# Performance work log

Measured on AMD Instinct MI355X. Metric: run time of the kernel, lower is better.

The kernel has to match this reference:

```python
import jax, jax.numpy as jnp
import numpy as np

# Video-DiT scale: d_model = H * D = 2048
B, S_T, S_C, H, D = 2, 2048, 1024, 16, 128


def setup_inputs() -> dict:
    key = jax.random.key(0)
    ks = jax.random.split(key, 6)
    f = lambda k, s: jax.random.normal(k, s, dtype=jnp.float32)
    return {
        "target_q": f(ks[0], (B, S_T, H, D)),
        "target_k": f(ks[1], (B, S_T, H, D)),
        "target_v": f(ks[2], (B, S_T, H, D)),
        "cond_k": f(ks[3], (B, S_C, H, D)),
        "cond_v": f(ks[4], (B, S_C, H, D)),
        "b_param": f(ks[5], (1,)),
    }


def reference(target_q, target_k, target_v, cond_k, cond_v, b_param):
    """Extended target self-attention over [target_k; cond_k] with a scalar
    logit bias b_param added only to the condition-key columns.
    Inputs BSHD; returns [B, S_t, H*D] (ready for output_proj)."""
    Bq, St, Hh, Dd = target_q.shape
    Sc = cond_k.shape[1]
    scale = Dd ** -0.5  # softmax_scale defaults to head_dim**-0.5

    k_ext = jnp.concatenate([target_k, cond_k], axis=1)  # [B, S_t+S_c, H, D]
    v_ext = jnp.concatenate([target_v, cond_v], axis=1)

    # [B, H, S_t, S_t+S_c]
    logits = jnp.einsum('bqhd,bkhd->bhqk', target_q, k_ext) * jnp.asarray(scale, target_q.dtype)
    # bias: 0 on target keys, b on cond keys
    bias = jnp.concatenate([
        jnp.zeros((St,), logits.dtype),
        jnp.broadcast_to(b_param.astype(logits.dtype), (Sc,)),
    ])
    logits = logits + bias[None, None, None, :]

    probs = jax.nn.softmax(logits, axis=-1)
    out = jnp.einsum('bhqk,bkhd->bqhd', probs, v_ext)  # [B, S_t, H, D]
    return out.reshape(Bq, St, Hh * Dd)
```

## Files before the change

kernel.cpp:

```cpp
#include <hip/hip_runtime.h>
#include <hip/hip_bf16.h>

typedef __attribute__((ext_vector_type(4))) float f32x4;
typedef __attribute__((ext_vector_type(16))) float f32x16;
typedef __attribute__((ext_vector_type(8))) short bf8;
typedef __attribute__((ext_vector_type(2))) int i32x2;

#define B_ 2
#define ST 2048
#define SC 1024
#define SK 3072
#define NH 16
#define DH 128
#define KVB 32
#define NT 96
#define TGT 64
#define SCALE 0.088388347648318447f
#define LOG2E 1.4426950408889634f
#define PRE_TILE_U32 2048
#define PRE_BYTES (32ull * 96 * 512 * 16)
#define WS_NEED (2ull * PRE_BYTES)

__device__ __forceinline__ i32x2 tr_read(unsigned a) {
    i32x2 d;
    asm volatile("ds_read_b64_tr_b16 %0, %1" : "=v"(d) : "v"(a));
    return d;
}

__device__ __forceinline__ unsigned cvtpk(float lo, float hi) {
    unsigned r;
    asm("v_cvt_pk_bf16_f32 %0, %1, %2" : "=v"(r) : "v"(lo), "v"(hi));
    return r;
}

__device__ __forceinline__ void swap32(unsigned &a, unsigned &b) {
    asm volatile("v_permlane32_swap_b32 %0, %1" : "+v"(a), "+v"(b));
}

__device__ __forceinline__ bf8 mk_bf8(i32x2 a, i32x2 b) {
    union { i32x2 h[2]; bf8 v; } u;
    u.h[0] = a; u.h[1] = b;
    return u.v;
}
__device__ __forceinline__ bf8 mk_bf8w(unsigned w0, unsigned w1, unsigned w2, unsigned w3) {
    union { unsigned w[4]; bf8 v; } u;
    u.w[0] = w0; u.w[1] = w1; u.w[2] = w2; u.w[3] = w3;
    return u.v;
}
__device__ __forceinline__ bf8 pack_bf8(f32x4 a, f32x4 b) {
    return mk_bf8w(cvtpk(a[0], a[1]), cvtpk(a[2], a[3]),
                   cvtpk(b[0], b[1]), cvtpk(b[2], b[3]));
}

__global__ __launch_bounds__(256)
void preconv(const float* __restrict__ TK, const float* __restrict__ TV,
             const float* __restrict__ CK, const float* __restrict__ CV,
             unsigned* __restrict__ KP, unsigned* __restrict__ VP)
{
    const unsigned gid = blockIdx.x * 256 + threadIdx.x;
    const int c    = gid & 511;
    const int idx  = gid >> 9;
    const int bhid = idx / 96;
    const int t    = idx - bhid * 96;
    const int bb   = bhid >> 4;
    const int hh   = bhid & 15;
    const int lc   = c & 63;
    const int r31c = lc & 31;
    const int hic  = lc >> 5;

    const bool tgt = (t < TGT);
    const size_t krowbase = tgt
        ? (((size_t)bb * ST + t * 32) * NH + hh) * DH
        : (((size_t)bb * SC + (t * 32 - ST)) * NH + hh) * DH;
    const float* kb = (tgt ? TK : CK) + krowbase;
    const float* vb = (tgt ? TV : CV) + krowbase;

    {
        const int dk = c >> 6;
        const float* kp = kb + (size_t)r31c * (NH * DH) + dk * 16 + hic * 8;
        const f32x4 k0 = *(const f32x4*)kp;
        const f32x4 k1 = *(const f32x4*)(kp + 4);
        unsigned* ko = KP + (size_t)gid * 4;
        ko[0] = cvtpk(k0[0], k0[1]); ko[1] = cvtpk(k0[2], k0[3]);
        ko[2] = cvtpk(k1[0], k1[1]); ko[3] = cvtpk(k1[2], k1[3]);
    }

    {
        const int s  = c >> 6;
        const int ks = s >> 2;
        const int dt = s & 3;
        const int d  = dt * 32 + r31c;
        const float* vp = vb + (size_t)(ks * 16 + hic * 8) * (NH * DH) + d;
        float vv[8];
#pragma unroll
        for (int j = 0; j < 8; ++j) vv[j] = vp[(size_t)j * (NH * DH)];
        unsigned* vo = VP + (size_t)gid * 4;
        vo[0] = cvtpk(vv[0], vv[1]); vo[1] = cvtpk(vv[2], vv[3]);
        vo[2] = cvtpk(vv[4], vv[5]); vo[3] = cvtpk(vv[6], vv[7]);
    }
}

__global__ __launch_bounds__(256) __attribute__((amdgpu_waves_per_eu(2, 2)))
void attn_fwd_pre(const float* __restrict__ Q,
                  const unsigned* __restrict__ KP,
                  const unsigned* __restrict__ VP,
                  const float* __restrict__ BP,
                  float* __restrict__ OUT)
{
    __shared__ __align__(16) unsigned short Ks[3][KVB * DH];
    __shared__ __align__(16) unsigned short Vs[3][KVB * DH];

    const int tid = threadIdx.x;
    const int w   = tid >> 6;
    const int l   = tid & 63;
    const int r31 = l & 31;
    const int hi  = l >> 5;

    const int bid = blockIdx.x;
    const int xcd = bid & 7;
    const int sub = bid >> 3;
    const int bh  = xcd * 4 + (sub >> 4);
    const int qt  = sub & 15;
    const int bb  = bh >> 4;
    const int hh  = bh & 15;
    const int bh96 = bh * 96;

    const float biasl = BP[0] * LOG2E;

    const int qrow = qt * 128 + w * 32 + r31;
    const float* qp = Q + (((size_t)bb * ST + qrow) * NH + hh) * DH;
    const float qsc = SCALE * LOG2E;
    bf8 qf[8];
#pragma unroll
    for (int dk = 0; dk < 8; ++dk) {
        const f32x4 x0 = *(const f32x4*)(qp + dk * 16 + hi * 8);
        const f32x4 x1 = *(const f32x4*)(qp + dk * 16 + hi * 8 + 4);
        qf[dk] = mk_bf8w(cvtpk(x0[0]*qsc, x0[1]*qsc), cvtpk(x0[2]*qsc, x0[3]*qsc),
                         cvtpk(x1[0]*qsc, x1[1]*qsc), cvtpk(x1[2]*qsc, x1[3]*qsc));
    }

    f32x16 oa[4];
#pragma unroll
    for (int dt = 0; dt < 4; ++dt)
#pragma unroll
        for (int e = 0; e < 16; ++e) oa[dt][e] = 0.f;
    float l_run = 0.f;

    auto stage = [&](int t, int buf) {
        const unsigned* kt = KP + (size_t)(bh96 + t) * PRE_TILE_U32;
        const unsigned* vt = VP + (size_t)(bh96 + t) * PRE_TILE_U32;
#pragma unroll
        for (int i = 0; i < 2; ++i) {
            const int cb = (w << 6) + (i << 8);
            const unsigned kdst = (unsigned)(size_t)&Ks[buf][cb * 8];
            const unsigned vdst = (unsigned)(size_t)&Vs[buf][cb * 8];
            const unsigned* kg = kt + (size_t)(cb + l) * 4;
            const unsigned* vg = vt + (size_t)(cb + l) * 4;
            __builtin_amdgcn_global_load_lds(
                (const __attribute__((address_space(1))) unsigned*)(size_t)kg,
                (__attribute__((address_space(3))) unsigned*)(size_t)kdst, 16, 0, 0);
            __builtin_amdgcn_global_load_lds(
                (const __attribute__((address_space(1))) unsigned*)(size_t)vg,
                (__attribute__((address_space(3))) unsigned*)(size_t)vdst, 16, 0, 0);
        }
    };

    const char* kLane = (const char*)&Ks[0][0] + l * 16;
    const char* vLane = (const char*)&Vs[0][0] + l * 16;

    auto qk_into = [&](f32x16& SN, int bufn, float biasn) {
#pragma unroll
        for (int e = 0; e < 16; ++e) SN[e] = biasn;
        const char* kB = kLane + (unsigned)bufn * 8192u;
        __builtin_amdgcn_s_setprio(1);
#pragma unroll
        for (int dk = 0; dk < 8; ++dk) {
            const bf8 kf = *(const bf8*)(kB + dk * 1024);
            SN = __builtin_amdgcn_mfma_f32_32x32x16_bf16(kf, qf[dk], SN, 0, 0, 0);
        }
        __builtin_amdgcn_s_setprio(0);
    };

    stage(0, 0);
    stage(1, 1);
    asm volatile("s_waitcnt vmcnt(4)" ::: "memory");
    __builtin_amdgcn_s_barrier();
    asm volatile("" ::: "memory");
    f32x16 sA, sB;
    qk_into(sA, 0, 0.f);

    int b0 = 0, b1 = 1, b2 = 2;

    auto body = [&](int t, f32x16& SCr, f32x16& SNr) {
        if (t + 1 < NT) asm volatile("s_waitcnt vmcnt(0)" ::: "memory");
        __builtin_amdgcn_s_barrier();
        asm volatile("" ::: "memory");
        if (t + 2 < NT) stage(t + 2, b2);

        if (t + 1 < NT)
            qk_into(SNr, b1, (t + 1 >= TGT) ? biasl : 0.f);

        const char* vB = vLane + (unsigned)b0 * 8192u;
        bf8 vf[8];
#pragma unroll
        for (int s = 0; s < 8; ++s)
            vf[s] = *(const bf8*)(vB + s * 1024);

        float rs = 0.f;
#pragma unroll
        for (int e = 0; e < 16; ++e) {
            SCr[e] = __builtin_amdgcn_exp2f(SCr[e]);
            rs += SCr[e];
        }
        l_run += rs;

        unsigned a0 = cvtpk(SCr[0], SCr[1]),  c0 = cvtpk(SCr[4], SCr[5]);
        unsigned a1 = cvtpk(SCr[2], SCr[3]),  c1 = cvtpk(SCr[6], SCr[7]);
        swap32(a0, c0); swap32(a1, c1);
        const bf8 pf0 = mk_bf8w(a0, a1, c0, c1);
        unsigned a2 = cvtpk(SCr[8], SCr[9]),   c2 = cvtpk(SCr[12], SCr[13]);
        unsigned a3 = cvtpk(SCr[10], SCr[11]), c3 = cvtpk(SCr[14], SCr[15]);
        swap32(a2, c2); swap32(a3, c3);
        const bf8 pf1 = mk_bf8w(a2, a3, c2, c3);

        __builtin_amdgcn_s_setprio(1);
#pragma unroll
        for (int dt = 0; dt < 4; ++dt)
            oa[dt] = __builtin_amdgcn_mfma_f32_32x32x16_bf16(vf[dt], pf0, oa[dt], 0, 0, 0);
#pragma unroll
        for (int dt = 0; dt < 4; ++dt)
            oa[dt] = __builtin_amdgcn_mfma_f32_32x32x16_bf16(vf[4 + dt], pf1, oa[dt], 0, 0, 0);
        __builtin_amdgcn_s_setprio(0);

        const int n0 = b1, n1 = b2, n2 = b0;
        b0 = n0; b1 = n1; b2 = n2;
    };

    for (int t = 0; t < NT; t += 2) {
        body(t, sA, sB);
        body(t + 1, sB, sA);
    }

    const float l_tot = l_run + __shfl_xor(l_run, 32);
    const float inv = 1.0f / l_tot;
    float* op = OUT + ((size_t)(bb * ST + qrow)) * (NH * DH) + hh * DH;
#pragma unroll
    for (int dt = 0; dt < 4; ++dt)
#pragma unroll
        for (int rr = 0; rr < 4; ++rr) {
            f32x4 st;
            st[0] = oa[dt][rr * 4 + 0] * inv;
            st[1] = oa[dt][rr * 4 + 1] * inv;
            st[2] = oa[dt][rr * 4 + 2] * inv;
            st[3] = oa[dt][rr * 4 + 3] * inv;
            *(f32x4*)(op + dt * 32 + rr * 8 + hi * 4) = st;
        }
}

__global__ __launch_bounds__(256, 2)
void attn_fwd_reg(const float* __restrict__ Q,
                  const float* __restrict__ TK,
                  const float* __restrict__ TV,
                  const float* __restrict__ CK,
                  const float* __restrict__ CV,
                  const float* __restrict__ BP,
                  float* __restrict__ OUT)
{
    __shared__ __align__(16) unsigned short Ks[2][KVB * DH];
    __shared__ __align__(16) unsigned short Vs[2][KVB * DH];

    const int tid = threadIdx.x;
    const int w   = tid >> 6;
    const int l   = tid & 63;
    const int r31 = l & 31;
    const int hi  = l >> 5;

    const int bid = blockIdx.x;
    const int xcd = bid & 7;
    const int sub = bid >> 3;
    const int bh  = xcd * 4 + (sub >> 4);
    const int qt  = sub & 15;
    const int bb  = bh >> 4;
    const int hh  = bh & 15;

    const float biasl = BP[0] * LOG2E;

    const int qrow = qt * 128 + w * 32 + r31;
    const float* qp = Q + (((size_t)bb * ST + qrow) * NH + hh) * DH;
    const float qsc = SCALE * LOG2E;
    bf8 qf[8];
#pragma unroll
    for (int dk = 0; dk < 8; ++dk) {
        const f32x4 x0 = *(const f32x4*)(qp + dk * 16 + hi * 8);
        const f32x4 x1 = *(const f32x4*)(qp + dk * 16 + hi * 8 + 4);
        qf[dk] = mk_bf8w(cvtpk(x0[0]*qsc, x0[1]*qsc), cvtpk(x0[2]*qsc, x0[3]*qsc),
                         cvtpk(x1[0]*qsc, x1[1]*qsc), cvtpk(x1[2]*qsc, x1[3]*qsc));
    }

    f32x16 oa[4];
#pragma unroll
    for (int dt = 0; dt < 4; ++dt)
#pragma unroll
        for (int e = 0; e < 16; ++e) oa[dt][e] = 0.f;
    float l_run = 0.f;

    f32x4 skr[2][2], svr[2][2];

    auto stage_load = [&](int t) {
        const int kv0 = t * KVB;
        const float *kb, *vb;
        if (kv0 < ST) {
            const size_t off = (((size_t)bb * ST + kv0) * NH + hh) * DH;
            kb = TK + off; vb = TV + off;
        } else {
            const size_t off = (((size_t)bb * SC + (kv0 - ST)) * NH + hh) * DH;
            kb = CK + off; vb = CV + off;
        }
#pragma unroll
        for (int i = 0; i < 2; ++i) {
            const int c = tid + (i << 8);
            const int krow = c >> 4;
            const int kcol = ((c & 15) ^ (krow & 7)) << 3;
            const float* kp = kb + (size_t)krow * (NH * DH) + kcol;
            skr[i][0] = *(const f32x4*)kp;
            skr[i][1] = *(const f32x4*)(kp + 4);
            const int vkv = (((c >> 8) & 1) << 4) | (((c >> 4) & 1) << 3)
                          | (((c >> 7) & 1) << 2) | ((c >> 1) & 3);
            const int vd  = (((c >> 5) & 3) << 5) | (((c >> 3) & 1) << 4)
                          | ((c & 1) << 3);
            const float* vp = vb + (size_t)vkv * (NH * DH) + vd;
            svr[i][0] = *(const f32x4*)vp;
            svr[i][1] = *(const f32x4*)(vp + 4);
        }
    };
    auto stage_write = [&](int buf) {
#pragma unroll
        for (int i = 0; i < 2; ++i) {
            const int c = tid + (i << 8);
            *(bf8*)((char*)Ks[buf] + c * 16) = pack_bf8(skr[i][0], skr[i][1]);
            *(bf8*)((char*)Vs[buf] + c * 16) = pack_bf8(svr[i][0], svr[i][1]);
        }
    };

    stage_load(0);
    stage_write(0);

    const unsigned vLane = (unsigned)(size_t)&Vs[0][0]
                         + (unsigned)((l >> 4) * 128 + (l & 15) * 8);

    for (int t = 0; t < NT; ++t) {
        __syncthreads();
        if (t + 1 < NT) stage_load(t + 1);
        const int buf = t & 1;
        const float bias = (t >= TGT) ? biasl : 0.f;

        f32x16 s0;
#pragma unroll
        for (int e = 0; e < 16; ++e) s0[e] = bias;
        __builtin_amdgcn_s_setprio(1);
#pragma unroll
        for (int dk = 0; dk < 8; ++dk) {
            int o = r31 * 256 + (dk * 16 + hi * 8) * 2;
            o ^= (r31 & 7) << 4;
            const bf8 kf = *(const bf8*)((const char*)Ks[buf] + o);
            s0 = __builtin_amdgcn_mfma_f32_32x32x16_bf16(kf, qf[dk], s0, 0, 0, 0);
        }
        __builtin_amdgcn_s_setprio(0);

        asm volatile("" ::: "memory");
        const unsigned vA = vLane + (unsigned)(buf << 13);
        i32x2 vt_[2][4][2];
#pragma unroll
        for (int ks = 0; ks < 2; ++ks) {
            const unsigned vk = vA + (unsigned)(ks << 12);
#pragma unroll
            for (int dt = 0; dt < 4; ++dt) {
                vt_[ks][dt][0] = tr_read(vk + dt * 512);
                vt_[ks][dt][1] = tr_read(vk + dt * 512 + 2048);
            }
        }

        if (t + 1 < NT) stage_write(buf ^ 1);

        float rs = 0.f;
#pragma unroll
        for (int e = 0; e < 16; ++e) {
            s0[e] = __builtin_amdgcn_exp2f(s0[e]);
            rs += s0[e];
        }
        l_run += rs;

        unsigned a0 = cvtpk(s0[0], s0[1]),  b0 = cvtpk(s0[4], s0[5]);
        unsigned a1 = cvtpk(s0[2], s0[3]),  b1 = cvtpk(s0[6], s0[7]);
        swap32(a0, b0); swap32(a1, b1);
        const bf8 pf0 = mk_bf8w(a0, a1, b0, b1);
        unsigned a2 = cvtpk(s0[8], s0[9]),   b2 = cvtpk(s0[12], s0[13]);
        unsigned a3 = cvtpk(s0[10], s0[11]), b3 = cvtpk(s0[14], s0[15]);
        swap32(a2, b2); swap32(a3, b3);
        const bf8 pf1 = mk_bf8w(a2, a3, b2, b3);

        asm volatile("s_waitcnt lgkmcnt(0)");
        __builtin_amdgcn_sched_barrier(0);
        __builtin_amdgcn_s_setprio(1);
#pragma unroll
        for (int ks = 0; ks < 2; ++ks) {
            const bf8 pf = ks ? pf1 : pf0;
#pragma unroll
            for (int dt = 0; dt < 4; ++dt) {
                const bf8 vf = mk_bf8(vt_[ks][dt][0], vt_[ks][dt][1]);
                oa[dt] = __builtin_amdgcn_mfma_f32_32x32x16_bf16(vf, pf, oa[dt], 0, 0, 0);
            }
        }
        __builtin_amdgcn_s_setprio(0);
    }

    const float l_tot = l_run + __shfl_xor(l_run, 32);
    const float inv = 1.0f / l_tot;
    float* op = OUT + ((size_t)(bb * ST + qrow)) * (NH * DH) + hh * DH;
#pragma unroll
    for (int dt = 0; dt < 4; ++dt)
#pragma unroll
        for (int rr = 0; rr < 4; ++rr) {
            f32x4 st;
            st[0] = oa[dt][rr * 4 + 0] * inv;
            st[1] = oa[dt][rr * 4 + 1] * inv;
            st[2] = oa[dt][rr * 4 + 2] * inv;
            st[3] = oa[dt][rr * 4 + 3] * inv;
            *(f32x4*)(op + dt * 32 + rr * 8 + hi * 4) = st;
        }
}

extern "C" void kernel_launch(void* const* d_in, const int* in_sizes, int n_in,
                              void* d_out, int out_size, void* d_ws, size_t ws_size,
                              hipStream_t stream) {
    const float* q  = (const float*)d_in[0];
    const float* tk = (const float*)d_in[1];
    const float* tv = (const float*)d_in[2];
    const float* ck = (const float*)d_in[3];
    const float* cv = (const float*)d_in[4];
    const float* bp = (const float*)d_in[5];
    float* out = (float*)d_out;

    if (ws_size >= WS_NEED) {
        unsigned* kp = (unsigned*)d_ws;
        unsigned* vp = (unsigned*)((char*)d_ws + PRE_BYTES);
        preconv<<<dim3(6144), 256, 0, stream>>>(tk, tv, ck, cv, kp, vp);
        attn_fwd_pre<<<dim3(512), 256, 0, stream>>>(q, kp, vp, bp, out);
    } else {
        attn_fwd_reg<<<dim3(512), 256, 0, stream>>>(q, tk, tv, ck, cv, bp, out);
    }
}
```

Baseline: 139.0 us.

## Load prepacked K/V tiles directly into registers, bypassing LDS staging

Removes the triple-buffered LDS staging of K/V tiles (global_load_lds plus block barriers). Each wave now reads the prepacked bf16 K and V fragments straight from global memory into registers, prefetching the next K tile one iteration ahead. The aim is to cut barrier synchronisation and LDS traffic. In exchange, each of the four waves loads the same tiles, which multiplies cache traffic. The V load latency and the QK-to-softmax dependency are also less hidden, since QK is no longer computed one tile ahead.

```diff
diff --git a/kernel.cpp b/kernel.cpp
--- a/kernel.cpp
+++ b/kernel.cpp
@@ -107,9 +107,6 @@
                   const float* __restrict__ BP,
                   float* __restrict__ OUT)
 {
-    __shared__ __align__(16) unsigned short Ks[3][KVB * DH];
-    __shared__ __align__(16) unsigned short Vs[3][KVB * DH];
-
     const int tid = threadIdx.x;
     const int w   = tid >> 6;
     const int l   = tid & 63;
@@ -146,99 +143,70 @@
         for (int e = 0; e < 16; ++e) oa[dt][e] = 0.f;
     float l_run = 0.f;
 
-    auto stage = [&](int t, int buf) {
-        const unsigned* kt = KP + (size_t)(bh96 + t) * PRE_TILE_U32;
-        const unsigned* vt = VP + (size_t)(bh96 + t) * PRE_TILE_U32;
-#pragma unroll
-        for (int i = 0; i < 2; ++i) {
-            const int cb = (w << 6) + (i << 8);
-            const unsigned kdst = (unsigned)(size_t)&Ks[buf][cb * 8];
-            const unsigned vdst = (unsigned)(size_t)&Vs[buf][cb * 8];
-            const unsigned* kg = kt + (size_t)(cb + l) * 4;
-            const unsigned* vg = vt + (size_t)(cb + l) * 4;
-            __builtin_amdgcn_global_load_lds(
-                (const __attribute__((address_space(1))) unsigned*)(size_t)kg,
-                (__attribute__((address_space(3))) unsigned*)(size_t)kdst, 16, 0, 0);
-            __builtin_amdgcn_global_load_lds(
-                (const __attribute__((address_space(1))) unsigned*)(size_t)vg,
-                (__attribute__((address_space(3))) unsigned*)(size_t)vdst, 16, 0, 0);
-        }
-    };
-
-    const char* kLane = (const char*)&Ks[0][0] + l * 16;
-    const char* vLane = (const char*)&Vs[0][0] + l * 16;
-
-    auto qk_into = [&](f32x16& SN, int bufn, float biasn) {
-#pragma unroll
-        for (int e = 0; e < 16; ++e) SN[e] = biasn;
-        const char* kB = kLane + (unsigned)bufn * 8192u;
+    const char* kBase = (const char*)KP + (size_t)bh96 * 8192 + (size_t)l * 16;
+    const char* vBase = (const char*)VP + (size_t)bh96 * 8192 + (size_t)l * 16;
+
+    bf8 kA[8], kB[8], vC[8];
+
+    {
+        const char* kt = kBase;
+#pragma unroll
+        for (int i = 0; i < 8; ++i)
+            kA[i] = *(const bf8*)(kt + i * 1024);
+    }
+
+    auto body = [&](int t, bf8* kCur, bf8* kNext) {
+        const char* vt = vBase + (size_t)t * 8192;
+#pragma unroll
+        for (int i = 0; i < 8; ++i)
+            vC[i] = *(const bf8*)(vt + i * 1024);
+        if (t + 1 < NT) {
+            const char* kt = kBase + (size_t)(t + 1) * 8192;
+#pragma unroll
+            for (int i = 0; i < 8; ++i)
+                kNext[i] = *(const bf8*)(kt + i * 1024);
+        }
+
+        const float bias = (t >= TGT) ? biasl : 0.f;
+        f32x16 s;
+#pragma unroll
+        for (int e = 0; e < 16; ++e) s[e] = bias;
         __builtin_amdgcn_s_setprio(1);
 #pragma unroll
-        for (int dk = 0; dk < 8; ++dk) {
-            const bf8 kf = *(const bf8*)(kB + dk * 1024);
-            SN = __builtin_amdgcn_mfma_f32_32x32x16_bf16(kf, qf[dk], SN, 0, 0, 0);
-        }
+        for (int dk = 0; dk < 8; ++dk)
+            s = __builtin_amdgcn_mfma_f32_32x32x16_bf16(kCur[dk], qf[dk], s, 0, 0, 0);
+        __builtin_amdgcn_s_setprio(0);
+
+        float rs = 0.f;
+#pragma unroll
+        for (int e = 0; e < 16; ++e) {
+            s[e] = __builtin_amdgcn_exp2f(s[e]);
+            rs += s[e];
+        }
+        l_run += rs;
+
+        unsigned a0 = cvtpk(s[0], s[1]),  c0 = cvtpk(s[4], s[5]);
+        unsigned a1 = cvtpk(s[2], s[3]),  c1 = cvtpk(s[6], s[7]);
+        swap32(a0, c0); swap32(a1, c1);
+        const bf8 pf0 = mk_bf8w(a0, a1, c0, c1);
+        unsigned a2 = cvtpk(s[8], s[9]),   c2 = cvtpk(s[12], s[13]);
+        unsigned a3 = cvtpk(s[10], s[11]), c3 = cvtpk(s[14], s[15]);
+        swap32(a2, c2); swap32(a3, c3);
+        const bf8 pf1 = mk_bf8w(a2, a3, c2, c3);
+
+        __builtin_amdgcn_s_setprio(1);
+#pragma unroll
+        for (int dt = 0; dt < 4; ++dt)
+            oa[dt] = __builtin_amdgcn_mfma_f32_32x32x16_bf16(vC[dt], pf0, oa[dt], 0, 0, 0);
+#pragma unroll
+        for (int dt = 0; dt < 4; ++dt)
+            oa[dt] = __builtin_amdgcn_mfma_f32_32x32x16_bf16(vC[4 + dt], pf1, oa[dt], 0, 0, 0);
         __builtin_amdgcn_s_setprio(0);
     };
 
-    stage(0, 0);
-    stage(1, 1);
-    asm volatile("s_waitcnt vmcnt(4)" ::: "memory");
-    __builtin_amdgcn_s_barrier();
-    asm volatile("" ::: "memory");
-    f32x16 sA, sB;
-    qk_into(sA, 0, 0.f);
-
-    int b0 = 0, b1 = 1, b2 = 2;
-
-    auto body = [&](int t, f32x16& SCr, f32x16& SNr) {
-        if (t + 1 < NT) asm volatile("s_waitcnt vmcnt(0)" ::: "memory");
-        __builtin_amdgcn_s_barrier();
-        asm volatile("" ::: "memory");
-        if (t + 2 < NT) stage(t + 2, b2);
-
-        if (t + 1 < NT)
-            qk_into(SNr, b1, (t + 1 >= TGT) ? biasl : 0.f);
-
-        const char* vB = vLane + (unsigned)b0 * 8192u;
-        bf8 vf[8];
-#pragma unroll
-        for (int s = 0; s < 8; ++s)
-            vf[s] = *(const bf8*)(vB + s * 1024);
-
-        float rs = 0.f;
-#pragma unroll
-        for (int e = 0; e < 16; ++e) {
-            SCr[e] = __builtin_amdgcn_exp2f(SCr[e]);
-            rs += SCr[e];
-        }
-        l_run += rs;
-
-        unsigned a0 = cvtpk(SCr[0], SCr[1]),  c0 = cvtpk(SCr[4], SCr[5]);
-        unsigned a1 = cvtpk(SCr[2], SCr[3]),  c1 = cvtpk(SCr[6], SCr[7]);
-        swap32(a0, c0); swap32(a1, c1);
-        const bf8 pf0 = mk_bf8w(a0, a1, c0, c1);
-        unsigned a2 = cvtpk(SCr[8], SCr[9]),   c2 = cvtpk(SCr[12], SCr[13]);
-        unsigned a3 = cvtpk(SCr[10], SCr[11]), c3 = cvtpk(SCr[14], SCr[15]);
-        swap32(a2, c2); swap32(a3, c3);
-        const bf8 pf1 = mk_bf8w(a2, a3, c2, c3);
-
-        __builtin_amdgcn_s_setprio(1);
-#pragma unroll
-        for (int dt = 0; dt < 4; ++dt)
-            oa[dt] = __builtin_amdgcn_mfma_f32_32x32x16_bf16(vf[dt], pf0, oa[dt], 0, 0, 0);
-#pragma unroll
-        for (int dt = 0; dt < 4; ++dt)
-            oa[dt] = __builtin_amdgcn_mfma_f32_32x32x16_bf16(vf[4 + dt], pf1, oa[dt], 0, 0, 0);
-        __builtin_amdgcn_s_setprio(0);
-
-        const int n0 = b1, n1 = b2, n2 = b0;
-        b0 = n0; b1 = n1; b2 = n2;
-    };
-
     for (int t = 0; t < NT; t += 2) {
-        body(t, sA, sB);
-        body(t + 1, sB, sA);
+        body(t, kA, kB);
+        body(t + 1, kB, kA);
     }
 
     const float l_tot = l_run + __shfl_xor(l_run, 32);
```

Measured after the change: 163.9 us. +17.9%, slower.
